# Performance work log

Hardware: AMD Instinct MI355X
Metric: run time of the kernel (lower is better)

Reference implementation:

```python
import jax, jax.numpy as jnp
import numpy as np

N_USERS = 50000
N_ENT = 150000
N = N_USERS + N_ENT
E = 2000000
B = 8192
DIMS = [64, 64, 32, 16]  # emb_dim + weight_size


def _xavier(k, shape):
    fi, fo = (shape[0], shape[1]) if len(shape) == 2 else (1, shape[-1])
    lim = float(np.sqrt(6.0 / (fi + fo)))
    return jax.random.uniform(k, shape, jnp.float32, -lim, lim)


def setup_inputs() -> dict:
    key = jax.random.key(0)
    ks = jax.random.split(key, 32)
    inp = {}
    inp["users"] = jax.random.randint(ks[0], (B,), 0, N_USERS)
    inp["pos_items"] = jax.random.randint(ks[1], (B,), 0, N_ENT)
    inp["neg_items"] = jax.random.randint(ks[2], (B,), 0, N_ENT)
    inp["rows"] = jax.random.randint(ks[3], (E,), 0, N)
    inp["cols"] = jax.random.randint(ks[4], (E,), 0, N)
    # attentive normalized adjacency values (softmax-normalized in KGAT, ~1/degree scale)
    inp["edge_vals"] = jax.random.uniform(ks[5], (E,), jnp.float32) / 10.0
    inp["user_embed"] = _xavier(ks[6], (N_USERS, DIMS[0]))
    inp["entity_embed"] = _xavier(ks[7], (N_ENT, DIMS[0]))
    i = 8
    for l in range(3):
        din, dout = DIMS[l], DIMS[l + 1]
        inp[f"W_gc{l}"] = _xavier(ks[i], (din, dout)); i += 1
        inp[f"b_gc{l}"] = _xavier(ks[i], (1, dout)); i += 1
        inp[f"W_bi{l}"] = _xavier(ks[i], (din, dout)); i += 1
        inp[f"b_bi{l}"] = _xavier(ks[i], (1, dout)); i += 1
    return inp


def _l2norm(x):
    # F.normalize(x, p=2, dim=1)
    return x / jnp.maximum(jnp.linalg.norm(x, axis=1, keepdims=True), 1e-12)


def reference(users, pos_items, neg_items, rows, cols, edge_vals, user_embed, entity_embed,
              W_gc0, b_gc0, W_bi0, b_bi0, W_gc1, b_gc1, W_bi1, b_bi1, W_gc2, b_gc2, W_bi2, b_bi2):
    ego = jnp.concatenate([user_embed, entity_embed], axis=0)  # [N, 64]
    layer_params = [(W_gc0, b_gc0, W_bi0, b_bi0),
                    (W_gc1, b_gc1, W_bi1, b_bi1),
                    (W_gc2, b_gc2, W_bi2, b_bi2)]
    embs = [ego]
    for Wg, bg, Wb, bb in layer_params:
        # side = A_in @ ego  (sparse COO matmul as gather + segment_sum)
        side = jax.ops.segment_sum(edge_vals[:, None] * ego[cols], rows, num_segments=N)
        sum_emb = jax.nn.leaky_relu((ego + side) @ Wg + bg)  # bi-interaction sum branch
        bi_emb = jax.nn.leaky_relu((ego * side) @ Wb + bb)   # bi-interaction elementwise branch
        ego = sum_emb + bi_emb
        embs.append(_l2norm(ego))
    all_emb = jnp.concatenate(embs, axis=1)  # [N, 64+64+32+16]
    ua, ea = all_emb[:N_USERS], all_emb[N_USERS:]
    u_e = ua[users]
    pos_i_e = ea[pos_items]
    neg_i_e = ea[neg_items]
    pos_scores = jnp.sum(u_e * pos_i_e, axis=1)
    neg_scores = jnp.sum(u_e * neg_i_e, axis=1)
    return jnp.stack([pos_scores, neg_scores], axis=-1)  # [B, 2]
```

## Files before the change

kernel.cpp:

```cpp
#include <hip/hip_runtime.h>

#define N_USERS 50000
#define N_ENT   150000
#define N_NODES 200000
#define NE      2000000
#define BATCH   8192

#define BSHIFT 9
#define BROWS  512
#define NBUK   391
#define EPB    8192
#define PBLK   245
#define T0_BLKS 12500
#define WT_BLKS 52

typedef __attribute__((ext_vector_type(8))) short   bf16x8;
typedef __attribute__((ext_vector_type(4))) float   f32x4;
typedef unsigned int u32;

__device__ __forceinline__ float bf2f(unsigned short b) {
    return __uint_as_float(((u32)b) << 16);
}
__device__ __forceinline__ float bflo(u32 x) {
    return __uint_as_float(x << 16);
}
__device__ __forceinline__ float bfhi(u32 x) {
    return __uint_as_float(x & 0xFFFF0000u);
}
__device__ __forceinline__ unsigned short f2bf(float f) {
    u32 u = __float_as_uint(f);
    u += 0x7FFF + ((u >> 16) & 1);
    return (unsigned short)(u >> 16);
}
__device__ __forceinline__ u32 cvtpk(float lo, float hi) {
    u32 r;
    asm("v_cvt_pk_bf16_f32 %0, %1, %2" : "=v"(r) : "v"(lo), "v"(hi));
    return r;
}

__global__ __launch_bounds__(256) void bhist(const int4* __restrict__ rows4,
                                             int* __restrict__ bcnt) {
    __shared__ int lcnt[NBUK];
    for (int b = threadIdx.x; b < NBUK; b += 256) lcnt[b] = 0;
    __syncthreads();
    const int q0 = blockIdx.x * (EPB / 4);
#pragma unroll
    for (int k = 0; k < EPB / 1024; ++k) {
        int q = q0 + k * 256 + threadIdx.x;
        if (q < NE / 4) {
            int4 r = rows4[q];
            atomicAdd(&lcnt[r.x >> BSHIFT], 1);
            atomicAdd(&lcnt[r.y >> BSHIFT], 1);
            atomicAdd(&lcnt[r.z >> BSHIFT], 1);
            atomicAdd(&lcnt[r.w >> BSHIFT], 1);
        }
    }
    __syncthreads();
    for (int b = threadIdx.x; b < NBUK; b += 256) {
        int c = lcnt[b];
        if (c) atomicAdd(&bcnt[b], c);
    }
}

__global__ __launch_bounds__(512) void bscan(const int* __restrict__ bcnt,
                                             int* __restrict__ bsc,
                                             int* __restrict__ gcur) {
    __shared__ int buf[512];
    int t = threadIdx.x;
    int v = (t < NBUK) ? bcnt[t] : 0;
    buf[t] = v;
    __syncthreads();
    for (int off = 1; off < 512; off <<= 1) {
        int x = (t >= off) ? buf[t - off] : 0;
        __syncthreads();
        buf[t] += x;
        __syncthreads();
    }
    if (t < NBUK) {
        int excl = buf[t] - v;
        bsc[t]  = excl;
        gcur[t] = excl;
    }
    if (t == NBUK - 1) bsc[NBUK] = buf[t];
}

__global__ __launch_bounds__(256) void part_kernel(const int4* __restrict__ rows4,
                                                   const int4* __restrict__ cols4,
                                                   const float4* __restrict__ vals4,
                                                   int* __restrict__ gcur,
                                                   uint2* __restrict__ part) {
    __shared__ int lcnt[NBUK];
    __shared__ int lbase[NBUK];
    for (int b = threadIdx.x; b < NBUK; b += 256) lcnt[b] = 0;
    __syncthreads();
    const int q0 = blockIdx.x * (EPB / 4);
    int4 rc[EPB / 1024];
#pragma unroll
    for (int k = 0; k < EPB / 1024; ++k) {
        int q = q0 + k * 256 + threadIdx.x;
        if (q < NE / 4) {
            int4 r = rows4[q];
            rc[k] = r;
            atomicAdd(&lcnt[r.x >> BSHIFT], 1);
            atomicAdd(&lcnt[r.y >> BSHIFT], 1);
            atomicAdd(&lcnt[r.z >> BSHIFT], 1);
            atomicAdd(&lcnt[r.w >> BSHIFT], 1);
        } else {
            rc[k] = make_int4(-1, -1, -1, -1);
        }
    }
    __syncthreads();
    for (int b = threadIdx.x; b < NBUK; b += 256) {
        int c = lcnt[b];
        lbase[b] = c ? atomicAdd(&gcur[b], c) : 0;
        lcnt[b] = 0;
    }
    __syncthreads();
#pragma unroll
    for (int k = 0; k < EPB / 1024; ++k) {
        int q = q0 + k * 256 + threadIdx.x;
        if (q < NE / 4) {
            int4   c4 = cols4[q];
            float4 v4 = vals4[q];
            int r, b, rk;
            uint2 rec;
            r = rc[k].x; b = r >> BSHIFT; rk = atomicAdd(&lcnt[b], 1);
            rec.x = ((u32)(r & (BROWS - 1)) << 18) | (u32)c4.x;
            rec.y = __float_as_uint(v4.x);  part[lbase[b] + rk] = rec;
            r = rc[k].y; b = r >> BSHIFT; rk = atomicAdd(&lcnt[b], 1);
            rec.x = ((u32)(r & (BROWS - 1)) << 18) | (u32)c4.y;
            rec.y = __float_as_uint(v4.y);  part[lbase[b] + rk] = rec;
            r = rc[k].z; b = r >> BSHIFT; rk = atomicAdd(&lcnt[b], 1);
            rec.x = ((u32)(r & (BROWS - 1)) << 18) | (u32)c4.z;
            rec.y = __float_as_uint(v4.z);  part[lbase[b] + rk] = rec;
            r = rc[k].w; b = r >> BSHIFT; rk = atomicAdd(&lcnt[b], 1);
            rec.x = ((u32)(r & (BROWS - 1)) << 18) | (u32)c4.w;
            rec.y = __float_as_uint(v4.w);  part[lbase[b] + rk] = rec;
        }
    }
}

__global__ __launch_bounds__(512) void bfill(const uint2* __restrict__ part,
                                             const int* __restrict__ bsc,
                                             int* __restrict__ rs,
                                             int* __restrict__ deg,
                                             uint2* __restrict__ ep) {
    __shared__ int h[BROWS];
    __shared__ int sc[BROWS];
    const int b = blockIdx.x;
    const int t = threadIdx.x;
    const int s = bsc[b];
    const int e = bsc[b + 1];
    h[t] = 0;
    __syncthreads();
    for (int i = s + t; i < e; i += 512)
        atomicAdd(&h[part[i].x >> 18], 1);
    __syncthreads();
    int v = h[t];
    sc[t] = v;
    __syncthreads();
    for (int off = 1; off < 512; off <<= 1) {
        int x = (t >= off) ? sc[t - off] : 0;
        __syncthreads();
        sc[t] += x;
        __syncthreads();
    }
    const int row = b * BROWS + t;
    if (row < N_NODES) {
        deg[row] = v;
        rs[row]  = s + sc[t];
    }
    h[t] = s + sc[t] - v;
    __syncthreads();
    for (int i = s + t; i < e; i += 512) {
        uint2 rec = part[i];
        int lr  = rec.x >> 18;
        int pos = atomicAdd(&h[lr], 1);
        uint2 o;
        o.x = rec.x & 0x3FFFF;
        o.y = rec.y;
        ep[pos] = o;
    }
}

__global__ __launch_bounds__(256) void init_misc(
        const float* __restrict__ ue, const float* __restrict__ ee,
        unsigned short* __restrict__ t0,
        const float* __restrict__ Wg0, const float* __restrict__ Wb0,
        const float* __restrict__ Wg1, const float* __restrict__ Wb1,
        const float* __restrict__ Wg2, const float* __restrict__ Wb2,
        unsigned short* __restrict__ wt) {
    if (blockIdx.x < T0_BLKS) {
        int i = blockIdx.x * 256 + threadIdx.x;
        const int uelems = N_USERS * 64 / 4;
        float4 v = (i < uelems) ? ((const float4*)ue)[i]
                                : ((const float4*)ee)[i - uelems];
        ushort4 o;
        o.x = f2bf(v.x); o.y = f2bf(v.y); o.z = f2bf(v.z); o.w = f2bf(v.w);
        ((ushort4*)t0)[i] = o;
        return;
    }
    int idx = (blockIdx.x - T0_BLKS) * 256 + threadIdx.x;
    if (idx < 4096) {
        int k = idx >> 6, n = idx & 63;
        wt[0 + n * 64 + k] = f2bf(Wg0[idx]);
    } else if (idx < 8192) {
        int r = idx - 4096; int k = r >> 6, n = r & 63;
        wt[4096 + n * 64 + k] = f2bf(Wb0[r]);
    } else if (idx < 10240) {
        int r = idx - 8192; int k = r >> 5, n = r & 31;
        wt[8192 + n * 64 + k] = f2bf(Wg1[r]);
    } else if (idx < 12288) {
        int r = idx - 10240; int k = r >> 5, n = r & 31;
        wt[10240 + n * 64 + k] = f2bf(Wb1[r]);
    } else if (idx < 12800) {
        int r = idx - 12288; int k = r >> 4, n = r & 15;
        wt[12288 + n * 32 + k] = f2bf(Wg2[r]);
    } else if (idx < 13312) {
        int r = idx - 12800; int k = r >> 4, n = r & 15;
        wt[12800 + n * 32 + k] = f2bf(Wb2[r]);
    }
}

template <int DIN, int DOUT, int EGO, int WX>
__global__ __launch_bounds__(256) void layer_fused(
        const int* __restrict__ rs, const int* __restrict__ deg,
        const uint2* __restrict__ ep,
        const unsigned short* __restrict__ tin,
        const float* __restrict__ ue, const float* __restrict__ ee,
        const float* __restrict__ xin,
        const unsigned short* __restrict__ WgT,
        const unsigned short* __restrict__ WbT,
        const float* __restrict__ bg, const float* __restrict__ bb,
        float* __restrict__ xout,
        unsigned short* __restrict__ tout,
        float* __restrict__ norm_out) {
    constexpr int NTC = DOUT / 16;
    constexpr int R   = (4 / NTC) * 16;
    constexpr int RPW = R / 4;
    constexpr int KS  = DIN / 32;

    __shared__ __align__(16) unsigned short sH[R * DIN];
    __shared__ __align__(16) unsigned short sP[R * DIN];
    __shared__ float sPart[R * NTC];

    const int lane    = threadIdx.x & 63;
    const int wave    = threadIdx.x >> 6;
    const int rowbase = blockIdx.x * R;

    for (int rr = 0; rr < RPW; ++rr) {
        const int lr  = wave * RPW + rr;
        const int row = __builtin_amdgcn_readfirstlane(rowbase + lr);
        const int end   = rs[row];
        const int start = end - deg[row];

        if (DIN == 64) {
            const int g  = lane >> 5;
            const int d2 = lane & 31;
            const u32* t32 = (const u32*)tin;
            float ax0 = 0.f, ax1 = 0.f, ax2 = 0.f, ax3 = 0.f;
            float ay0 = 0.f, ay1 = 0.f, ay2 = 0.f, ay3 = 0.f;
            for (int i = start; i < end; i += 16) {
                const int rem = end - i;
                uint2 q0  = ep[i + 0],  q1  = ep[i + 1];
                uint2 q2  = ep[i + 2],  q3  = ep[i + 3];
                uint2 q4  = ep[i + 4],  q5  = ep[i + 5];
                uint2 q6  = ep[i + 6],  q7  = ep[i + 7];
                uint2 q8  = ep[i + 8],  q9  = ep[i + 9];
                uint2 q10 = ep[i + 10], q11 = ep[i + 11];
                uint2 q12 = ep[i + 12], q13 = ep[i + 13];
                uint2 q14 = ep[i + 14], q15 = ep[i + 15];
                u32 m0  = (0  < rem) ? q0.x  : 0u;  u32 w0  = (0  < rem) ? q0.y  : 0u;
                u32 m1  = (1  < rem) ? q1.x  : 0u;  u32 w1  = (1  < rem) ? q1.y  : 0u;
                u32 m2  = (2  < rem) ? q2.x  : 0u;  u32 w2  = (2  < rem) ? q2.y  : 0u;
                u32 m3  = (3  < rem) ? q3.x  : 0u;  u32 w3  = (3  < rem) ? q3.y  : 0u;
                u32 m4  = (4  < rem) ? q4.x  : 0u;  u32 w4  = (4  < rem) ? q4.y  : 0u;
                u32 m5  = (5  < rem) ? q5.x  : 0u;  u32 w5  = (5  < rem) ? q5.y  : 0u;
                u32 m6  = (6  < rem) ? q6.x  : 0u;  u32 w6  = (6  < rem) ? q6.y  : 0u;
                u32 m7  = (7  < rem) ? q7.x  : 0u;  u32 w7  = (7  < rem) ? q7.y  : 0u;
                u32 m8  = (8  < rem) ? q8.x  : 0u;  u32 w8  = (8  < rem) ? q8.y  : 0u;
                u32 m9  = (9  < rem) ? q9.x  : 0u;  u32 w9  = (9  < rem) ? q9.y  : 0u;
                u32 m10 = (10 < rem) ? q10.x : 0u;  u32 w10 = (10 < rem) ? q10.y : 0u;
                u32 m11 = (11 < rem) ? q11.x : 0u;  u32 w11 = (11 < rem) ? q11.y : 0u;
                u32 m12 = (12 < rem) ? q12.x : 0u;  u32 w12 = (12 < rem) ? q12.y : 0u;
                u32 m13 = (13 < rem) ? q13.x : 0u;  u32 w13 = (13 < rem) ? q13.y : 0u;
                u32 m14 = (14 < rem) ? q14.x : 0u;  u32 w14 = (14 < rem) ? q14.y : 0u;
                u32 m15 = (15 < rem) ? q15.x : 0u;  u32 w15 = (15 < rem) ? q15.y : 0u;
                u32 s0 = g ? m1  : m0;   float v0 = __uint_as_float(g ? w1  : w0);
                u32 s1 = g ? m3  : m2;   float v1 = __uint_as_float(g ? w3  : w2);
                u32 s2 = g ? m5  : m4;   float v2 = __uint_as_float(g ? w5  : w4);
                u32 s3 = g ? m7  : m6;   float v3 = __uint_as_float(g ? w7  : w6);
                u32 s4 = g ? m9  : m8;   float v4 = __uint_as_float(g ? w9  : w8);
                u32 s5 = g ? m11 : m10;  float v5 = __uint_as_float(g ? w11 : w10);
                u32 s6 = g ? m13 : m12;  float v6 = __uint_as_float(g ? w13 : w12);
                u32 s7 = g ? m15 : m14;  float v7 = __uint_as_float(g ? w15 : w14);
                u32 x0 = t32[(size_t)s0 * 32 + d2];
                u32 x1 = t32[(size_t)s1 * 32 + d2];
                u32 x2 = t32[(size_t)s2 * 32 + d2];
                u32 x3 = t32[(size_t)s3 * 32 + d2];
                u32 x4 = t32[(size_t)s4 * 32 + d2];
                u32 x5 = t32[(size_t)s5 * 32 + d2];
                u32 x6 = t32[(size_t)s6 * 32 + d2];
                u32 x7 = t32[(size_t)s7 * 32 + d2];
                ax0 = fmaf(v0, bflo(x0), ax0);  ay0 = fmaf(v0, bfhi(x0), ay0);
                ax1 = fmaf(v1, bflo(x1), ax1);  ay1 = fmaf(v1, bfhi(x1), ay1);
                ax2 = fmaf(v2, bflo(x2), ax2);  ay2 = fmaf(v2, bfhi(x2), ay2);
                ax3 = fmaf(v3, bflo(x3), ax3);  ay3 = fmaf(v3, bfhi(x3), ay3);
                ax0 = fmaf(v4, bflo(x4), ax0);  ay0 = fmaf(v4, bfhi(x4), ay0);
                ax1 = fmaf(v5, bflo(x5), ax1);  ay1 = fmaf(v5, bfhi(x5), ay1);
                ax2 = fmaf(v6, bflo(x6), ax2);  ay2 = fmaf(v6, bfhi(x6), ay2);
                ax3 = fmaf(v7, bflo(x7), ax3);  ay3 = fmaf(v7, bfhi(x7), ay3);
            }
            float ax = (ax0 + ax1) + (ax2 + ax3);
            float ay = (ay0 + ay1) + (ay2 + ay3);
            ax += __shfl_xor(ax, 32);
            ay += __shfl_xor(ay, 32);

            float ex, ey;
            if (EGO == 0) {
                const float2* src = (row < N_USERS)
                    ? (const float2*)ue + (size_t)row * 32
                    : (const float2*)ee + (size_t)(row - N_USERS) * 32;
                float2 ev = src[d2];  ex = ev.x;  ey = ev.y;
            } else if (EGO == 1) {
                float2 ev = ((const float2*)xin)[(size_t)row * 32 + d2];
                ex = ev.x;  ey = ev.y;
            } else {
                u32 tv = t32[(size_t)row * 32 + d2];
                ex = bflo(tv);  ey = bfhi(tv);
            }
            if (g == 0) {
                ((u32*)sH)[lr * 32 + d2] = cvtpk(ex + ax, ey + ay);
                ((u32*)sP)[lr * 32 + d2] = cvtpk(ex * ax, ey * ay);
            }
        } else {
            const int g  = lane >> 4;
            const int d2 = lane & 15;
            const u32* t16 = (const u32*)tin;
            float ax0 = 0.f, ax1 = 0.f;
            float ay0 = 0.f, ay1 = 0.f;
            for (int i = start; i < end; i += 16) {
                const int rem = end - i;
                uint2 q0  = ep[i + 0],  q1  = ep[i + 1];
                uint2 q2  = ep[i + 2],  q3  = ep[i + 3];
                uint2 q4  = ep[i + 4],  q5  = ep[i + 5];
                uint2 q6  = ep[i + 6],  q7  = ep[i + 7];
                uint2 q8  = ep[i + 8],  q9  = ep[i + 9];
                uint2 q10 = ep[i + 10], q11 = ep[i + 11];
                uint2 q12 = ep[i + 12], q13 = ep[i + 13];
                uint2 q14 = ep[i + 14], q15 = ep[i + 15];
                u32 m0  = (0  < rem) ? q0.x  : 0u;  u32 w0  = (0  < rem) ? q0.y  : 0u;
                u32 m1  = (1  < rem) ? q1.x  : 0u;  u32 w1  = (1  < rem) ? q1.y  : 0u;
                u32 m2  = (2  < rem) ? q2.x  : 0u;  u32 w2  = (2  < rem) ? q2.y  : 0u;
                u32 m3  = (3  < rem) ? q3.x  : 0u;  u32 w3  = (3  < rem) ? q3.y  : 0u;
                u32 m4  = (4  < rem) ? q4.x  : 0u;  u32 w4  = (4  < rem) ? q4.y  : 0u;
                u32 m5  = (5  < rem) ? q5.x  : 0u;  u32 w5  = (5  < rem) ? q5.y  : 0u;
                u32 m6  = (6  < rem) ? q6.x  : 0u;  u32 w6  = (6  < rem) ? q6.y  : 0u;
                u32 m7  = (7  < rem) ? q7.x  : 0u;  u32 w7  = (7  < rem) ? q7.y  : 0u;
                u32 m8  = (8  < rem) ? q8.x  : 0u;  u32 w8  = (8  < rem) ? q8.y  : 0u;
                u32 m9  = (9  < rem) ? q9.x  : 0u;  u32 w9  = (9  < rem) ? q9.y  : 0u;
                u32 m10 = (10 < rem) ? q10.x : 0u;  u32 w10 = (10 < rem) ? q10.y : 0u;
                u32 m11 = (11 < rem) ? q11.x : 0u;  u32 w11 = (11 < rem) ? q11.y : 0u;
                u32 m12 = (12 < rem) ? q12.x : 0u;  u32 w12 = (12 < rem) ? q12.y : 0u;
                u32 m13 = (13 < rem) ? q13.x : 0u;  u32 w13 = (13 < rem) ? q13.y : 0u;
                u32 m14 = (14 < rem) ? q14.x : 0u;  u32 w14 = (14 < rem) ? q14.y : 0u;
                u32 m15 = (15 < rem) ? q15.x : 0u;  u32 w15 = (15 < rem) ? q15.y : 0u;
                u32 ta, tb; float fa, fb;
                ta = (g & 1) ? m1  : m0;   tb = (g & 1) ? m3  : m2;
                fa = __uint_as_float((g & 1) ? w1  : w0);
                fb = __uint_as_float((g & 1) ? w3  : w2);
                u32 s0 = (g & 2) ? tb : ta;  float v0 = (g & 2) ? fb : fa;
                ta = (g & 1) ? m5  : m4;   tb = (g & 1) ? m7  : m6;
                fa = __uint_as_float((g & 1) ? w5  : w4);
                fb = __uint_as_float((g & 1) ? w7  : w6);
                u32 s1 = (g & 2) ? tb : ta;  float v1 = (g & 2) ? fb : fa;
                ta = (g & 1) ? m9  : m8;   tb = (g & 1) ? m11 : m10;
                fa = __uint_as_float((g & 1) ? w9  : w8);
                fb = __uint_as_float((g & 1) ? w11 : w10);
                u32 s2 = (g & 2) ? tb : ta;  float v2 = (g & 2) ? fb : fa;
                ta = (g & 1) ? m13 : m12;  tb = (g & 1) ? m15 : m14;
                fa = __uint_as_float((g & 1) ? w13 : w12);
                fb = __uint_as_float((g & 1) ? w15 : w14);
                u32 s3 = (g & 2) ? tb : ta;  float v3 = (g & 2) ? fb : fa;
                u32 x0 = t16[(size_t)s0 * 16 + d2];
                u32 x1 = t16[(size_t)s1 * 16 + d2];
                u32 x2 = t16[(size_t)s2 * 16 + d2];
                u32 x3 = t16[(size_t)s3 * 16 + d2];
                ax0 = fmaf(v0, bflo(x0), ax0);  ay0 = fmaf(v0, bfhi(x0), ay0);
                ax1 = fmaf(v1, bflo(x1), ax1);  ay1 = fmaf(v1, bfhi(x1), ay1);
                ax0 = fmaf(v2, bflo(x2), ax0);  ay0 = fmaf(v2, bfhi(x2), ay0);
                ax1 = fmaf(v3, bflo(x3), ax1);  ay1 = fmaf(v3, bfhi(x3), ay1);
            }
            float ax = ax0 + ax1;
            float ay = ay0 + ay1;
            ax += __shfl_xor(ax, 32);  ay += __shfl_xor(ay, 32);
            ax += __shfl_xor(ax, 16);  ay += __shfl_xor(ay, 16);

            float ex, ey;
            if (EGO == 2) {
                u32 tv = t16[(size_t)row * 16 + d2];
                ex = bflo(tv);  ey = bfhi(tv);
            } else if (EGO == 1) {
                float2 ev = ((const float2*)xin)[(size_t)row * 16 + d2];
                ex = ev.x;  ey = ev.y;
            } else {
                const float2* src = (row < N_USERS)
                    ? (const float2*)ue + (size_t)row * 32
                    : (const float2*)ee + (size_t)(row - N_USERS) * 32;
                float2 ev = src[d2];  ex = ev.x;  ey = ev.y;
            }
            if (g == 0) {
                ((u32*)sH)[lr * 16 + d2] = cvtpk(ex + ax, ey + ay);
                ((u32*)sP)[lr * 16 + d2] = cvtpk(ex * ax, ey * ay);
            }
        }
    }
    __syncthreads();

    const int ct  = wave % NTC;
    const int rt  = wave / NTC;
    const int r16 = lane & 15;
    const int g4  = lane >> 4;

    bf16x8 ah[KS], ap[KS];
#pragma unroll
    for (int s = 0; s < KS; ++s) {
        const int aoff = (rt * 16 + r16) * DIN + g4 * 8 + s * 32;
        ah[s] = *reinterpret_cast<const bf16x8*>(sH + aoff);
        ap[s] = *reinterpret_cast<const bf16x8*>(sP + aoff);
    }
    f32x4 accg = (f32x4){0.f, 0.f, 0.f, 0.f};
    f32x4 accb = (f32x4){0.f, 0.f, 0.f, 0.f};
#pragma unroll
    for (int s = 0; s < KS; ++s) {
        const int boff = (ct * 16 + r16) * DIN + g4 * 8 + s * 32;
        bf16x8 bgf = *reinterpret_cast<const bf16x8*>(WgT + boff);
        bf16x8 bbf = *reinterpret_cast<const bf16x8*>(WbT + boff);
        accg = __builtin_amdgcn_mfma_f32_16x16x32_bf16(ah[s], bgf, accg, 0, 0, 0);
        accb = __builtin_amdgcn_mfma_f32_16x16x32_bf16(ap[s], bbf, accb, 0, 0, 0);
    }

    const int col = ct * 16 + r16;
    const float bgv = bg[col];
    const float bbv = bb[col];
    float ss[4];
#pragma unroll
    for (int r = 0; r < 4; ++r) {
        float a = accg[r] + bgv; a = a > 0.f ? a : 0.01f * a;
        float b = accb[r] + bbv; b = b > 0.f ? b : 0.01f * b;
        float nv = a + b;
        const int row = rowbase + rt * 16 + g4 * 4 + r;
        if (WX) xout[(size_t)row * DOUT + col] = nv;
        tout[(size_t)row * DOUT + col] = f2bf(nv);
        ss[r] = nv * nv;
    }
#pragma unroll
    for (int off = 1; off < 16; off <<= 1) {
#pragma unroll
        for (int r = 0; r < 4; ++r) ss[r] += __shfl_xor(ss[r], off);
    }
    if (r16 == 0) {
#pragma unroll
        for (int r = 0; r < 4; ++r)
            sPart[(rt * 16 + g4 * 4 + r) * NTC + ct] = ss[r];
    }
    __syncthreads();
    for (int t = threadIdx.x; t < R; t += 256) {
        float s = 0.f;
#pragma unroll
        for (int j = 0; j < NTC; ++j) s += sPart[t * NTC + j];
        norm_out[rowbase + t] = fmaxf(sqrtf(s), 1e-12f);
    }
}

__global__ __launch_bounds__(256) void score_kernel(
        const int* __restrict__ users, const int* __restrict__ pos,
        const int* __restrict__ neg,
        const float* __restrict__ ue, const float* __restrict__ ee,
        const float* __restrict__ e1, const float* __restrict__ n0,
        const unsigned short* __restrict__ t2, const float* __restrict__ n1,
        const unsigned short* __restrict__ t3, const float* __restrict__ n2,
        float* __restrict__ out) {
    int gid  = blockIdx.x * 256 + threadIdx.x;
    int idx  = gid >> 6;
    int lane = gid & 63;
    if (idx >= BATCH) return;
    int u  = users[idx];
    int pe = pos[idx];
    int ne = neg[idx];
    int pn = N_USERS + pe;
    int nn = N_USERS + ne;

    float s1p = 1.0f / (n0[u] * n0[pn]);
    float s1n = 1.0f / (n0[u] * n0[nn]);
    float s2p = 1.0f / (n1[u] * n1[pn]);
    float s2n = 1.0f / (n1[u] * n1[nn]);
    float s3p = 1.0f / (n2[u] * n2[pn]);
    float s3n = 1.0f / (n2[u] * n2[nn]);

    float ap = 0.f, an = 0.f;
    {
        float xu = ue[(size_t)u * 64 + lane];
        ap += xu * ee[(size_t)pe * 64 + lane];
        an += xu * ee[(size_t)ne * 64 + lane];
    }
    {
        float xu = e1[(size_t)u * 64 + lane];
        ap += xu * e1[(size_t)pn * 64 + lane] * s1p;
        an += xu * e1[(size_t)nn * 64 + lane] * s1n;
    }
    if (lane < 32) {
        float xu = bf2f(t2[(size_t)u * 32 + lane]);
        ap += xu * bf2f(t2[(size_t)pn * 32 + lane]) * s2p;
        an += xu * bf2f(t2[(size_t)nn * 32 + lane]) * s2n;
    } else if (lane < 48) {
        int d = lane - 32;
        float xu = bf2f(t3[(size_t)u * 16 + d]);
        ap += xu * bf2f(t3[(size_t)pn * 16 + d]) * s3p;
        an += xu * bf2f(t3[(size_t)nn * 16 + d]) * s3n;
    }
#pragma unroll
    for (int off = 32; off > 0; off >>= 1) {
        ap += __shfl_xor(ap, off);
        an += __shfl_xor(an, off);
    }
    if (lane == 0) {
        out[2 * idx + 0] = ap;
        out[2 * idx + 1] = an;
    }
}

extern "C" void kernel_launch(void* const* d_in, const int* in_sizes, int n_in,
                              void* d_out, int out_size, void* d_ws, size_t ws_size,
                              hipStream_t stream) {
    const int*   users = (const int*)d_in[0];
    const int*   pos   = (const int*)d_in[1];
    const int*   neg   = (const int*)d_in[2];
    const int*   rows  = (const int*)d_in[3];
    const int*   cols  = (const int*)d_in[4];
    const float* vals  = (const float*)d_in[5];
    const float* ue    = (const float*)d_in[6];
    const float* ee    = (const float*)d_in[7];
    const float* Wg0 = (const float*)d_in[8],  *bg0 = (const float*)d_in[9];
    const float* Wb0 = (const float*)d_in[10], *bb0 = (const float*)d_in[11];
    const float* Wg1 = (const float*)d_in[12], *bg1 = (const float*)d_in[13];
    const float* Wb1 = (const float*)d_in[14], *bb1 = (const float*)d_in[15];
    const float* Wg2 = (const float*)d_in[16], *bg2 = (const float*)d_in[17];
    const float* Wb2 = (const float*)d_in[18], *bb2 = (const float*)d_in[19];

    float* e1   = (float*)d_ws;
    float* n0   = e1 + (size_t)N_NODES * 64;
    float* n1   = n0 + N_NODES;
    float* n2   = n1 + N_NODES;
    uint2* ep   = (uint2*)(n2 + N_NODES);
    unsigned short* tA = (unsigned short*)(ep + NE);
    unsigned short* tB = tA + (size_t)N_NODES * 64;
    unsigned short* t3 = tB + (size_t)N_NODES * 64;
    unsigned short* wt = t3 + (size_t)N_NODES * 16;
    int* deg  = (int*)(wt + 13312);
    int* rs   = deg + N_NODES;
    int* bcnt = rs + N_NODES;
    int* bsc  = bcnt + NBUK;
    int* gcur = bsc + NBUK + 1;
    uint2* part = (uint2*)e1;

    hipMemsetAsync(bcnt, 0, NBUK * sizeof(int), stream);
    bhist<<<PBLK, 256, 0, stream>>>((const int4*)rows, bcnt);
    bscan<<<1, 512, 0, stream>>>(bcnt, bsc, gcur);
    part_kernel<<<PBLK, 256, 0, stream>>>((const int4*)rows, (const int4*)cols,
                                          (const float4*)vals, gcur, part);
    bfill<<<NBUK, 512, 0, stream>>>(part, bsc, rs, deg, ep);
    init_misc<<<T0_BLKS + WT_BLKS, 256, 0, stream>>>(ue, ee, tA,
                                                     Wg0, Wb0, Wg1, Wb1, Wg2, Wb2, wt);

    layer_fused<64, 64, 0, 1><<<N_NODES / 16, 256, 0, stream>>>(
        rs, deg, ep, tA, ue, ee, nullptr, wt, wt + 4096, bg0, bb0, e1, tB, n0);
    layer_fused<64, 32, 1, 0><<<N_NODES / 32, 256, 0, stream>>>(
        rs, deg, ep, tB, ue, ee, e1, wt + 8192, wt + 10240, bg1, bb1, nullptr, tA, n1);
    layer_fused<32, 16, 2, 0><<<N_NODES / 64, 256, 0, stream>>>(
        rs, deg, ep, tA, ue, ee, nullptr, wt + 12288, wt + 12800, bg2, bb2, nullptr, t3, n2);

    score_kernel<<<(BATCH * 64) / 256, 256, 0, stream>>>(users, pos, neg, ue, ee,
                                                         e1, n0, tA, n1, t3, n2,
                                                         (float*)d_out);
}
```

Measured before the change: 400.7 us.

## Switch intermediate embeddings to fp16, drop fp32 layer-1 copy, fuse init into histogram

Converts all packed intermediate embeddings and weights from bf16 to fp16 and uses fp16 MFMA. The fp32 layer-1 output buffer is removed, so layer 2 and the scoring kernel read the half-precision copy instead. This cuts one N×64 fp32 write and several reads. The embedding/weight conversion kernel is merged into the histogram launch as extra blocks, saving a launch. The risk is fp16 overflow or underflow compared with bf16, and lost precision from no longer keeping layer-1 values in fp32.

```diff
diff --git a/kernel.cpp b/kernel.cpp
--- a/kernel.cpp
+++ b/kernel.cpp
@@ -14,32 +14,82 @@
 #define T0_BLKS 12500
 #define WT_BLKS 52
 
-typedef __attribute__((ext_vector_type(8))) short   bf16x8;
-typedef __attribute__((ext_vector_type(4))) float   f32x4;
+typedef __attribute__((ext_vector_type(8))) _Float16 f16x8;
+typedef __attribute__((ext_vector_type(4))) float    f32x4;
 typedef unsigned int u32;
 
-__device__ __forceinline__ float bf2f(unsigned short b) {
-    return __uint_as_float(((u32)b) << 16);
-}
-__device__ __forceinline__ float bflo(u32 x) {
-    return __uint_as_float(x << 16);
-}
-__device__ __forceinline__ float bfhi(u32 x) {
-    return __uint_as_float(x & 0xFFFF0000u);
-}
-__device__ __forceinline__ unsigned short f2bf(float f) {
-    u32 u = __float_as_uint(f);
-    u += 0x7FFF + ((u >> 16) & 1);
-    return (unsigned short)(u >> 16);
-}
-__device__ __forceinline__ u32 cvtpk(float lo, float hi) {
+__device__ __forceinline__ float hlo(u32 x) {
+    union { unsigned short s; _Float16 h; } c;
+    c.s = (unsigned short)x;
+    return (float)c.h;
+}
+__device__ __forceinline__ float hhi(u32 x) {
+    union { unsigned short s; _Float16 h; } c;
+    c.s = (unsigned short)(x >> 16);
+    return (float)c.h;
+}
+__device__ __forceinline__ float h2f(unsigned short s) {
+    union { unsigned short s; _Float16 h; } c;
+    c.s = s;
+    return (float)c.h;
+}
+__device__ __forceinline__ unsigned short f2h(float f) {
+    union { _Float16 h; unsigned short s; } c;
+    c.h = (_Float16)f;
+    return c.s;
+}
+__device__ __forceinline__ u32 pkh(float lo, float hi) {
     u32 r;
-    asm("v_cvt_pk_bf16_f32 %0, %1, %2" : "=v"(r) : "v"(lo), "v"(hi));
+    asm("v_cvt_pkrtz_f16_f32 %0, %1, %2" : "=v"(r) : "v"(lo), "v"(hi));
     return r;
 }
 
 __global__ __launch_bounds__(256) void bhist(const int4* __restrict__ rows4,
-                                             int* __restrict__ bcnt) {
+                                             int* __restrict__ bcnt,
+                                             const float* __restrict__ ue,
+                                             const float* __restrict__ ee,
+                                             unsigned short* __restrict__ t0,
+                                             const float* __restrict__ Wg0,
+                                             const float* __restrict__ Wb0,
+                                             const float* __restrict__ Wg1,
+                                             const float* __restrict__ Wb1,
+                                             const float* __restrict__ Wg2,
+                                             const float* __restrict__ Wb2,
+                                             unsigned short* __restrict__ wt) {
+    if (blockIdx.x >= PBLK) {
+        int bi = blockIdx.x - PBLK;
+        if (bi < T0_BLKS) {
+            int i = bi * 256 + threadIdx.x;
+            const int uelems = N_USERS * 64 / 4;
+            float4 v = (i < uelems) ? ((const float4*)ue)[i]
+                                    : ((const float4*)ee)[i - uelems];
+            ushort4 o;
+            o.x = f2h(v.x); o.y = f2h(v.y); o.z = f2h(v.z); o.w = f2h(v.w);
+            ((ushort4*)t0)[i] = o;
+            return;
+        }
+        int idx = (bi - T0_BLKS) * 256 + threadIdx.x;
+        if (idx < 4096) {
+            int k = idx >> 6, n = idx & 63;
+            wt[0 + n * 64 + k] = f2h(Wg0[idx]);
+        } else if (idx < 8192) {
+            int r = idx - 4096; int k = r >> 6, n = r & 63;
+            wt[4096 + n * 64 + k] = f2h(Wb0[r]);
+        } else if (idx < 10240) {
+            int r = idx - 8192; int k = r >> 5, n = r & 31;
+            wt[8192 + n * 64 + k] = f2h(Wg1[r]);
+        } else if (idx < 12288) {
+            int r = idx - 10240; int k = r >> 5, n = r & 31;
+            wt[10240 + n * 64 + k] = f2h(Wb1[r]);
+        } else if (idx < 12800) {
+            int r = idx - 12288; int k = r >> 4, n = r & 15;
+            wt[12288 + n * 32 + k] = f2h(Wg2[r]);
+        } else if (idx < 13312) {
+            int r = idx - 12800; int k = r >> 4, n = r & 15;
+            wt[12800 + n * 32 + k] = f2h(Wb2[r]);
+        }
+        return;
+    }
     __shared__ int lcnt[NBUK];
     for (int b = threadIdx.x; b < NBUK; b += 256) lcnt[b] = 0;
     __syncthreads();
@@ -183,56 +233,15 @@
     }
 }
 
-__global__ __launch_bounds__(256) void init_misc(
-        const float* __restrict__ ue, const float* __restrict__ ee,
-        unsigned short* __restrict__ t0,
-        const float* __restrict__ Wg0, const float* __restrict__ Wb0,
-        const float* __restrict__ Wg1, const float* __restrict__ Wb1,
-        const float* __restrict__ Wg2, const float* __restrict__ Wb2,
-        unsigned short* __restrict__ wt) {
-    if (blockIdx.x < T0_BLKS) {
-        int i = blockIdx.x * 256 + threadIdx.x;
-        const int uelems = N_USERS * 64 / 4;
-        float4 v = (i < uelems) ? ((const float4*)ue)[i]
-                                : ((const float4*)ee)[i - uelems];
-        ushort4 o;
-        o.x = f2bf(v.x); o.y = f2bf(v.y); o.z = f2bf(v.z); o.w = f2bf(v.w);
-        ((ushort4*)t0)[i] = o;
-        return;
-    }
-    int idx = (blockIdx.x - T0_BLKS) * 256 + threadIdx.x;
-    if (idx < 4096) {
-        int k = idx >> 6, n = idx & 63;
-        wt[0 + n * 64 + k] = f2bf(Wg0[idx]);
-    } else if (idx < 8192) {
-        int r = idx - 4096; int k = r >> 6, n = r & 63;
-        wt[4096 + n * 64 + k] = f2bf(Wb0[r]);
-    } else if (idx < 10240) {
-        int r = idx - 8192; int k = r >> 5, n = r & 31;
-        wt[8192 + n * 64 + k] = f2bf(Wg1[r]);
-    } else if (idx < 12288) {
-        int r = idx - 10240; int k = r >> 5, n = r & 31;
-        wt[10240 + n * 64 + k] = f2bf(Wb1[r]);
-    } else if (idx < 12800) {
-        int r = idx - 12288; int k = r >> 4, n = r & 15;
-        wt[12288 + n * 32 + k] = f2bf(Wg2[r]);
-    } else if (idx < 13312) {
-        int r = idx - 12800; int k = r >> 4, n = r & 15;
-        wt[12800 + n * 32 + k] = f2bf(Wb2[r]);
-    }
-}
-
-template <int DIN, int DOUT, int EGO, int WX>
+template <int DIN, int DOUT, int EGO>
 __global__ __launch_bounds__(256) void layer_fused(
         const int* __restrict__ rs, const int* __restrict__ deg,
         const uint2* __restrict__ ep,
         const unsigned short* __restrict__ tin,
         const float* __restrict__ ue, const float* __restrict__ ee,
-        const float* __restrict__ xin,
         const unsigned short* __restrict__ WgT,
         const unsigned short* __restrict__ WbT,
         const float* __restrict__ bg, const float* __restrict__ bb,
-        float* __restrict__ xout,
         unsigned short* __restrict__ tout,
         float* __restrict__ norm_out) {
     constexpr int NTC = DOUT / 16;
@@ -302,14 +311,14 @@
                 u32 x5 = t32[(size_t)s5 * 32 + d2];
                 u32 x6 = t32[(size_t)s6 * 32 + d2];
                 u32 x7 = t32[(size_t)s7 * 32 + d2];
-                ax0 = fmaf(v0, bflo(x0), ax0);  ay0 = fmaf(v0, bfhi(x0), ay0);
-                ax1 = fmaf(v1, bflo(x1), ax1);  ay1 = fmaf(v1, bfhi(x1), ay1);
-                ax2 = fmaf(v2, bflo(x2), ax2);  ay2 = fmaf(v2, bfhi(x2), ay2);
-                ax3 = fmaf(v3, bflo(x3), ax3);  ay3 = fmaf(v3, bfhi(x3), ay3);
-                ax0 = fmaf(v4, bflo(x4), ax0);  ay0 = fmaf(v4, bfhi(x4), ay0);
-                ax1 = fmaf(v5, bflo(x5), ax1);  ay1 = fmaf(v5, bfhi(x5), ay1);
-                ax2 = fmaf(v6, bflo(x6), ax2);  ay2 = fmaf(v6, bfhi(x6), ay2);
-                ax3 = fmaf(v7, bflo(x7), ax3);  ay3 = fmaf(v7, bfhi(x7), ay3);
+                ax0 = fmaf(v0, hlo(x0), ax0);  ay0 = fmaf(v0, hhi(x0), ay0);
+                ax1 = fmaf(v1, hlo(x1), ax1);  ay1 = fmaf(v1, hhi(x1), ay1);
+                ax2 = fmaf(v2, hlo(x2), ax2);  ay2 = fmaf(v2, hhi(x2), ay2);
+                ax3 = fmaf(v3, hlo(x3), ax3);  ay3 = fmaf(v3, hhi(x3), ay3);
+                ax0 = fmaf(v4, hlo(x4), ax0);  ay0 = fmaf(v4, hhi(x4), ay0);
+                ax1 = fmaf(v5, hlo(x5), ax1);  ay1 = fmaf(v5, hhi(x5), ay1);
+                ax2 = fmaf(v6, hlo(x6), ax2);  ay2 = fmaf(v6, hhi(x6), ay2);
+                ax3 = fmaf(v7, hlo(x7), ax3);  ay3 = fmaf(v7, hhi(x7), ay3);
             }
             float ax = (ax0 + ax1) + (ax2 + ax3);
             float ay = (ay0 + ay1) + (ay2 + ay3);
@@ -322,16 +331,13 @@
                     ? (const float2*)ue + (size_t)row * 32
                     : (const float2*)ee + (size_t)(row - N_USERS) * 32;
                 float2 ev = src[d2];  ex = ev.x;  ey = ev.y;
-            } else if (EGO == 1) {
-                float2 ev = ((const float2*)xin)[(size_t)row * 32 + d2];
-                ex = ev.x;  ey = ev.y;
             } else {
                 u32 tv = t32[(size_t)row * 32 + d2];
-                ex = bflo(tv);  ey = bfhi(tv);
+                ex = hlo(tv);  ey = hhi(tv);
             }
             if (g == 0) {
-                ((u32*)sH)[lr * 32 + d2] = cvtpk(ex + ax, ey + ay);
-                ((u32*)sP)[lr * 32 + d2] = cvtpk(ex * ax, ey * ay);
+                ((u32*)sH)[lr * 32 + d2] = pkh(ex + ax, ey + ay);
+                ((u32*)sP)[lr * 32 + d2] = pkh(ex * ax, ey * ay);
             }
         } else {
             const int g  = lane >> 4;
@@ -386,10 +392,10 @@
                 u32 x1 = t16[(size_t)s1 * 16 + d2];
                 u32 x2 = t16[(size_t)s2 * 16 + d2];
                 u32 x3 = t16[(size_t)s3 * 16 + d2];
-                ax0 = fmaf(v0, bflo(x0), ax0);  ay0 = fmaf(v0, bfhi(x0), ay0);
-                ax1 = fmaf(v1, bflo(x1), ax1);  ay1 = fmaf(v1, bfhi(x1), ay1);
-                ax0 = fmaf(v2, bflo(x2), ax0);  ay0 = fmaf(v2, bfhi(x2), ay0);
-                ax1 = fmaf(v3, bflo(x3), ax1);  ay1 = fmaf(v3, bfhi(x3), ay1);
+                ax0 = fmaf(v0, hlo(x0), ax0);  ay0 = fmaf(v0, hhi(x0), ay0);
+                ax1 = fmaf(v1, hlo(x1), ax1);  ay1 = fmaf(v1, hhi(x1), ay1);
+                ax0 = fmaf(v2, hlo(x2), ax0);  ay0 = fmaf(v2, hhi(x2), ay0);
+                ax1 = fmaf(v3, hlo(x3), ax1);  ay1 = fmaf(v3, hhi(x3), ay1);
             }
             float ax = ax0 + ax1;
             float ay = ay0 + ay1;
@@ -397,21 +403,18 @@
             ax += __shfl_xor(ax, 16);  ay += __shfl_xor(ay, 16);
 
             float ex, ey;
-            if (EGO == 2) {
-                u32 tv = t16[(size_t)row * 16 + d2];
-                ex = bflo(tv);  ey = bfhi(tv);
-            } else if (EGO == 1) {
-                float2 ev = ((const float2*)xin)[(size_t)row * 16 + d2];
-                ex = ev.x;  ey = ev.y;
-            } else {
+            if (EGO == 0) {
                 const float2* src = (row < N_USERS)
                     ? (const float2*)ue + (size_t)row * 32
                     : (const float2*)ee + (size_t)(row - N_USERS) * 32;
                 float2 ev = src[d2];  ex = ev.x;  ey = ev.y;
+            } else {
+                u32 tv = t16[(size_t)row * 16 + d2];
+                ex = hlo(tv);  ey = hhi(tv);
             }
             if (g == 0) {
-                ((u32*)sH)[lr * 16 + d2] = cvtpk(ex + ax, ey + ay);
-                ((u32*)sP)[lr * 16 + d2] = cvtpk(ex * ax, ey * ay);
+                ((u32*)sH)[lr * 16 + d2] = pkh(ex + ax, ey + ay);
+                ((u32*)sP)[lr * 16 + d2] = pkh(ex * ax, ey * ay);
             }
         }
     }
@@ -422,22 +425,22 @@
     const int r16 = lane & 15;
     const int g4  = lane >> 4;
 
-    bf16x8 ah[KS], ap[KS];
+    f16x8 ah[KS], ap[KS];
 #pragma unroll
     for (int s = 0; s < KS; ++s) {
         const int aoff = (rt * 16 + r16) * DIN + g4 * 8 + s * 32;
-        ah[s] = *reinterpret_cast<const bf16x8*>(sH + aoff);
-        ap[s] = *reinterpret_cast<const bf16x8*>(sP + aoff);
+        ah[s] = *reinterpret_cast<const f16x8*>(sH + aoff);
+        ap[s] = *reinterpret_cast<const f16x8*>(sP + aoff);
     }
     f32x4 accg = (f32x4){0.f, 0.f, 0.f, 0.f};
     f32x4 accb = (f32x4){0.f, 0.f, 0.f, 0.f};
 #pragma unroll
     for (int s = 0; s < KS; ++s) {
         const int boff = (ct * 16 + r16) * DIN + g4 * 8 + s * 32;
-        bf16x8 bgf = *reinterpret_cast<const bf16x8*>(WgT + boff);
-        bf16x8 bbf = *reinterpret_cast<const bf16x8*>(WbT + boff);
-        accg = __builtin_amdgcn_mfma_f32_16x16x32_bf16(ah[s], bgf, accg, 0, 0, 0);
-        accb = __builtin_amdgcn_mfma_f32_16x16x32_bf16(ap[s], bbf, accb, 0, 0, 0);
+        f16x8 bgf = *reinterpret_cast<const f16x8*>(WgT + boff);
+        f16x8 bbf = *reinterpret_cast<const f16x8*>(WbT + boff);
+        accg = __builtin_amdgcn_mfma_f32_16x16x32_f16(ah[s], bgf, accg, 0, 0, 0);
+        accb = __builtin_amdgcn_mfma_f32_16x16x32_f16(ap[s], bbf, accb, 0, 0, 0);
     }
 
     const int col = ct * 16 + r16;
@@ -450,8 +453,7 @@
         float b = accb[r] + bbv; b = b > 0.f ? b : 0.01f * b;
         float nv = a + b;
         const int row = rowbase + rt * 16 + g4 * 4 + r;
-        if (WX) xout[(size_t)row * DOUT + col] = nv;
-        tout[(size_t)row * DOUT + col] = f2bf(nv);
+        tout[(size_t)row * DOUT + col] = f2h(nv);
         ss[r] = nv * nv;
     }
 #pragma unroll
@@ -477,7 +479,7 @@
         const int* __restrict__ users, const int* __restrict__ pos,
         const int* __restrict__ neg,
         const float* __restrict__ ue, const float* __restrict__ ee,
-        const float* __restrict__ e1, const float* __restrict__ n0,
+        const unsigned short* __restrict__ t1, const float* __restrict__ n0,
         const unsigned short* __restrict__ t2, const float* __restrict__ n1,
         const unsigned short* __restrict__ t3, const float* __restrict__ n2,
         float* __restrict__ out) {
@@ -505,19 +507,19 @@
         an += xu * ee[(size_t)ne * 64 + lane];
     }
     {
-        float xu = e1[(size_t)u * 64 + lane];
-        ap += xu * e1[(size_t)pn * 64 + lane] * s1p;
-        an += xu * e1[(size_t)nn * 64 + lane] * s1n;
+        float xu = h2f(t1[(size_t)u * 64 + lane]);
+        ap += xu * h2f(t1[(size_t)pn * 64 + lane]) * s1p;
+        an += xu * h2f(t1[(size_t)nn * 64 + lane]) * s1n;
     }
     if (lane < 32) {
-        float xu = bf2f(t2[(size_t)u * 32 + lane]);
-        ap += xu * bf2f(t2[(size_t)pn * 32 + lane]) * s2p;
-        an += xu * bf2f(t2[(size_t)nn * 32 + lane]) * s2n;
+        float xu = h2f(t2[(size_t)u * 32 + lane]);
+        ap += xu * h2f(t2[(size_t)pn * 32 + lane]) * s2p;
+        an += xu * h2f(t2[(size_t)nn * 32 + lane]) * s2n;
     } else if (lane < 48) {
         int d = lane - 32;
-        float xu = bf2f(t3[(size_t)u * 16 + d]);
-        ap += xu * bf2f(t3[(size_t)pn * 16 + d]) * s3p;
-        an += xu * bf2f(t3[(size_t)nn * 16 + d]) * s3n;
+        float xu = h2f(t3[(size_t)u * 16 + d]);
+        ap += xu * h2f(t3[(size_t)pn * 16 + d]) * s3p;
+        an += xu * h2f(t3[(size_t)nn * 16 + d]) * s3n;
     }
 #pragma unroll
     for (int off = 32; off > 0; off >>= 1) {
@@ -548,8 +550,7 @@
     const float* Wg2 = (const float*)d_in[16], *bg2 = (const float*)d_in[17];
     const float* Wb2 = (const float*)d_in[18], *bb2 = (const float*)d_in[19];
 
-    float* e1   = (float*)d_ws;
-    float* n0   = e1 + (size_t)N_NODES * 64;
+    float* n0   = (float*)d_ws;
     float* n1   = n0 + N_NODES;
     float* n2   = n1 + N_NODES;
     uint2* ep   = (uint2*)(n2 + N_NODES);
@@ -562,25 +563,25 @@
     int* bcnt = rs + N_NODES;
     int* bsc  = bcnt + NBUK;
     int* gcur = bsc + NBUK + 1;
-    uint2* part = (uint2*)e1;
+    uint2* part = (uint2*)(gcur + NBUK);
 
     hipMemsetAsync(bcnt, 0, NBUK * sizeof(int), stream);
-    bhist<<<PBLK, 256, 0, stream>>>((const int4*)rows, bcnt);
+    bhist<<<PBLK + T0_BLKS + WT_BLKS, 256, 0, stream>>>(
+        (const int4*)rows, bcnt, ue, ee, tA,
+        Wg0, Wb0, Wg1, Wb1, Wg2, Wb2, wt);
     bscan<<<1, 512, 0, stream>>>(bcnt, bsc, gcur);
     part_kernel<<<PBLK, 256, 0, stream>>>((const int4*)rows, (const int4*)cols,
                                           (const float4*)vals, gcur, part);
     bfill<<<NBUK, 512, 0, stream>>>(part, bsc, rs, deg, ep);
-    init_misc<<<T0_BLKS + WT_BLKS, 256, 0, stream>>>(ue, ee, tA,
-                                                     Wg0, Wb0, Wg1, Wb1, Wg2, Wb2, wt);
-
-    layer_fused<64, 64, 0, 1><<<N_NODES / 16, 256, 0, stream>>>(
-        rs, deg, ep, tA, ue, ee, nullptr, wt, wt + 4096, bg0, bb0, e1, tB, n0);
-    layer_fused<64, 32, 1, 0><<<N_NODES / 32, 256, 0, stream>>>(
-        rs, deg, ep, tB, ue, ee, e1, wt + 8192, wt + 10240, bg1, bb1, nullptr, tA, n1);
-    layer_fused<32, 16, 2, 0><<<N_NODES / 64, 256, 0, stream>>>(
-        rs, deg, ep, tA, ue, ee, nullptr, wt + 12288, wt + 12800, bg2, bb2, nullptr, t3, n2);
+
+    layer_fused<64, 64, 0><<<N_NODES / 16, 256, 0, stream>>>(
+        rs, deg, ep, tA, ue, ee, wt, wt + 4096, bg0, bb0, tB, n0);
+    layer_fused<64, 32, 2><<<N_NODES / 32, 256, 0, stream>>>(
+        rs, deg, ep, tB, ue, ee, wt + 8192, wt + 10240, bg1, bb1, tA, n1);
+    layer_fused<32, 16, 2><<<N_NODES / 64, 256, 0, stream>>>(
+        rs, deg, ep, tA, ue, ee, wt + 12288, wt + 12800, bg2, bb2, t3, n2);
 
     score_kernel<<<(BATCH * 64) / 256, 256, 0, stream>>>(users, pos, neg, ue, ee,
-                                                         e1, n0, tA, n1, t3, n2,
+                                                         tB, n0, tA, n1, t3, n2,
                                                          (float*)d_out);
 }
```

Result: no change. 394.0 us, median of 2 (-1.7%).
